# Kernel optimization log

Hardware: AMD Instinct MI355X
Metric: run time of the kernel (lower is better)

The kernel has to match this reference:

```python
import jax, jax.numpy as jnp
import numpy as np

D_MODEL = 2048
N_HEADS = 16
HEAD_DIM = D_MODEL // N_HEADS  # 128
MAX_T = 2048
ROPE_BASE = 10000.0


def _rope_tables(head_dim, max_t, base):
    inv = 1.0 / (base ** (np.arange(0, head_dim, 2, dtype=np.float32) / head_dim))
    t = np.arange(max_t, dtype=np.float32)
    fr = np.outer(t, inv)  # (T, head_dim//2)
    return jnp.asarray(np.cos(fr)), jnp.asarray(np.sin(fr))


def setup_inputs() -> dict:
    key = jax.random.key(0)
    k1, k2, k3 = jax.random.split(key, 3)
    B, T = 2, 2048
    x = jax.random.normal(k1, (B, T, D_MODEL), dtype=jnp.float32)
    Wqkv = jax.random.normal(k2, (3 * D_MODEL, D_MODEL), dtype=jnp.float32) * 0.02
    Wout = jax.random.normal(k3, (D_MODEL, D_MODEL), dtype=jnp.float32) * 0.02
    cos, sin = _rope_tables(HEAD_DIM, MAX_T, ROPE_BASE)
    rope_mask = jnp.arange(N_HEADS) < (N_HEADS // 2)  # first 8 heads RoPE, rest NoPE
    return {"x": x, "Wqkv": Wqkv, "Wout": Wout, "cos": cos, "sin": sin, "rope_mask": rope_mask}


def _apply_rope(t, cos, sin):
    # t: (B,H,T,hd); pairs are consecutive elements (x0,x1),(x2,x3),...
    B, H, T, hd = t.shape
    tr = t.reshape(B, H, T, hd // 2, 2)
    c = cos[:T][None, None, :, :]
    s = sin[:T][None, None, :, :]
    re = tr[..., 0] * c - tr[..., 1] * s
    im = tr[..., 0] * s + tr[..., 1] * c
    return jnp.stack([re, im], axis=-1).reshape(B, H, T, hd)


def reference(x, Wqkv, Wout, cos, sin, rope_mask):
    B, T, D = x.shape
    H = rope_mask.shape[0]
    hd = D // H
    qkv = x @ Wqkv.T  # (B,T,3D)
    q, k, v = jnp.split(qkv, 3, axis=-1)
    def heads(a):
        return a.reshape(B, T, H, hd).transpose(0, 2, 1, 3)  # (B,H,T,hd)
    q, k, v = heads(q), heads(k), heads(v)
    m = rope_mask[None, :, None, None]  # broadcast over (B,H,T,hd)
    q = jnp.where(m, _apply_rope(q, cos, sin), q)
    k = jnp.where(m, _apply_rope(k, cos, sin), k)
    scale = 1.0 / jnp.sqrt(jnp.asarray(hd, dtype=q.dtype))
    scores = jnp.einsum('bhtd,bhsd->bhts', q, k) * scale
    causal = jnp.tril(jnp.ones((T, T), dtype=bool))
    scores = jnp.where(causal[None, None], scores, jnp.asarray(-jnp.inf, dtype=scores.dtype))
    p = jax.nn.softmax(scores, axis=-1)
    out = jnp.einsum('bhts,bhsd->bhtd', p, v)
    out = out.transpose(0, 2, 1, 3).reshape(B, T, D)
    return out @ Wout.T
```

## Files before the change

### kernel.cpp

```cpp
#include <hip/hip_runtime.h>
#include <stdint.h>

typedef unsigned short u16;
typedef __attribute__((ext_vector_type(8))) short short8;
typedef __attribute__((ext_vector_type(4))) short s16x4;
typedef __attribute__((ext_vector_type(4))) float f32x4;
typedef __attribute__((ext_vector_type(16))) float f32x16;

__device__ __forceinline__ u16 f2bf(float f) {
  uint32_t x = __float_as_uint(f);
  x += 0x7fff + ((x >> 16) & 1);
  return (u16)(x >> 16);
}
__device__ __forceinline__ float bf2f(u16 u) {
  return __uint_as_float(((uint32_t)u) << 16);
}
__device__ __forceinline__ f32x4 mfma16(short8 a, short8 b, f32x4 c) {
  return __builtin_amdgcn_mfma_f32_16x16x32_bf16(a, b, c, 0, 0, 0);
}
__device__ __forceinline__ f32x16 mfma32(short8 a, short8 b, f32x16 c) {
  return __builtin_amdgcn_mfma_f32_32x32x16_bf16(a, b, c, 0, 0, 0);
}
__device__ __forceinline__ f32x4 mfma16k16(s16x4 a, s16x4 b, f32x4 c) {
  return __builtin_amdgcn_mfma_f32_16x16x16bf16_1k(a, b, c, 0, 0, 0);
}
__device__ __forceinline__ void gld16(const u16* g, u16* l) {
  __builtin_amdgcn_global_load_lds(
      (const __attribute__((address_space(1))) unsigned int*)g,
      (__attribute__((address_space(3))) unsigned int*)l, 16, 0, 0);
}
__device__ __forceinline__ float exp2a(float x) {
  float r;
  asm("v_exp_f32 %0, %1" : "=v"(r) : "v"(x));
  return r;
}

#define WAIT_VM(n) asm volatile("s_waitcnt vmcnt(" #n ")" ::: "memory")

__global__ __launch_bounds__(256) void cvt_all(const float* __restrict__ x,
                                               const float* __restrict__ wqkv,
                                               const float* __restrict__ wout,
                                               u16* __restrict__ xb,
                                               u16* __restrict__ wqkvb,
                                               u16* __restrict__ woutb) {
  long i = ((long)blockIdx.x * 256 + threadIdx.x) * 8;
  const float* s;
  u16* d;
  long off;
  if (i < 8388608) {
    s = x; d = xb; off = i;
  } else if (i < 20971520) {
    s = wqkv; d = wqkvb; off = i - 8388608;
  } else {
    s = wout; d = woutb; off = i - 20971520;
  }
  f32x4 a = *(const f32x4*)(s + off);
  f32x4 b = *(const f32x4*)(s + off + 4);
  short8 o;
#pragma unroll
  for (int j = 0; j < 4; j++) {
    o[j] = (short)f2bf(a[j]);
    o[j + 4] = (short)f2bf(b[j]);
  }
  *(short8*)(d + off) = o;
}

__global__ __launch_bounds__(512, 4) void gemm_qkv(const u16* __restrict__ A,
                                                   const u16* __restrict__ Bw,
                                                   u16* __restrict__ q3) {
  __shared__ __align__(16) u16 SA[12288];
  __shared__ __align__(16) u16 SB[18432];
  const int id = blockIdx.x;
  const int swz = (id & 7) * 128 + (id >> 3);
  const int by = swz & 31, bx = swz >> 5;
  const int m0 = by * 128, n0 = bx * 192;
  const int t = threadIdx.x, w = t >> 6, lane = t & 63;
  const int quad = lane >> 4, l15 = lane & 15;
  const int wm = w >> 2, wn = w & 3;
  const int rS = t >> 2, pS = t & 3;
  const int cS = (pS - (rS >> 1)) & 3;
  const size_t arowA = (size_t)(m0 + rS) * 2048 + cS * 8;
  const size_t arowB = (size_t)(n0 + rS) * 2048 + cS * 8;

  f32x4 acc[4][3] = {};
  const int pq = ((quad + (l15 >> 1)) & 3) * 8;

#define STAGE(KT, RS_)                                   \
  {                                                      \
    const u16* ga_ = A + arowA + (size_t)(KT) * 32;      \
    gld16(ga_, SA + (RS_)*4096 + t * 8);                 \
    const u16* gb_ = Bw + arowB + (size_t)(KT) * 32;     \
    u16* lb_ = SB + (RS_)*6144 + t * 8;                  \
    gld16(gb_, lb_);                                     \
    if (w < 4) gld16(gb_ + (size_t)128 * 2048, lb_ + 4096); \
  }

#define WAITQ                       \
  {                                 \
    if (w < 4) { WAIT_VM(3); }      \
    else       { WAIT_VM(2); }      \
  }

#define TILE(RC, RSS, TAU, DO_STAGE, WAIT)                                    \
  {                                                                           \
    const u16* Sa_ = SA + (RC)*4096;                                          \
    const u16* Sb_ = SB + (RC)*6144;                                          \
    if (DO_STAGE) STAGE((TAU) + 2, RSS);                                      \
    short8 af[4], bf[3];                                                      \
    _Pragma("unroll") for (int i = 0; i < 4; i++)                             \
        af[i] = *(const short8*)&Sa_[(wm * 64 + i * 16 + l15) * 32 + pq];     \
    _Pragma("unroll") for (int n = 0; n < 3; n++)                             \
        bf[n] = *(const short8*)&Sb_[(wn * 48 + n * 16 + l15) * 32 + pq];     \
    __builtin_amdgcn_s_setprio(1);                                            \
    _Pragma("unroll") for (int mi = 0; mi < 4; mi++)                          \
      _Pragma("unroll") for (int ni = 0; ni < 3; ni++)                        \
          acc[mi][ni] = mfma16(af[mi], bf[ni], acc[mi][ni]);                  \
    __builtin_amdgcn_s_setprio(0);                                            \
    WAIT;                                                                     \
    __builtin_amdgcn_s_barrier();                                             \
  }

  STAGE(0, 0);
  STAGE(1, 1);
  WAITQ;
  __builtin_amdgcn_s_barrier();

#pragma unroll 1
  for (int kt = 0; kt < 60; kt += 3) {
    TILE(0, 2, kt + 0, 1, WAITQ);
    TILE(1, 0, kt + 1, 1, WAITQ);
    TILE(2, 1, kt + 2, 1, WAITQ);
  }
  TILE(0, 2, 60, 1, WAITQ);
  TILE(1, 0, 61, 1, WAITQ);
  TILE(2, 1, 62, 0, WAIT_VM(0));
  TILE(0, 2, 63, 0, (void)0);
#undef TILE
#undef WAITQ
#undef STAGE

  const int bb = m0 >> 11, tt0 = m0 & 2047;
#pragma unroll
  for (int ni = 0; ni < 3; ni++) {
    const int gc = n0 + wn * 48 + ni * 16 + l15;
    const int which = gc >> 11;
    const int hh = (gc & 2047) >> 7, di = gc & 127;
    if (which == 2) {
      u16* vb = q3 + 16777216 + ((size_t)(bb * 16 + hh) * 128 + di) * 2048;
#pragma unroll
      for (int mi = 0; mi < 4; mi++) {
        const int tloc = tt0 + wm * 64 + mi * 16 + quad * 4;
        s16x4 st;
#pragma unroll
        for (int r = 0; r < 4; r++) st[r] = (short)f2bf(acc[mi][ni][r]);
        *(s16x4*)(vb + tloc) = st;
      }
    } else {
      const float sc = (which == 0) ? 0.1275174f : 1.0f;
      u16* qb = q3 + (size_t)which * 8388608 +
                ((size_t)(bb * 16 + hh) * 2048) * 128 + di;
#pragma unroll
      for (int mi = 0; mi < 4; mi++) {
        const int tloc = tt0 + wm * 64 + mi * 16 + quad * 4;
#pragma unroll
        for (int r = 0; r < 4; r++)
          qb[(size_t)(tloc + r) * 128] = f2bf(acc[mi][ni][r] * sc);
      }
    }
  }
}

template <int EPI>
__global__ __launch_bounds__(256) void gemm_bt(const u16* __restrict__ A,
                                               const u16* __restrict__ B,
                                               int K, void* __restrict__ Cv, int N) {
  __shared__ __align__(16) u16 SMEM[8448];
  u16* As = SMEM;
  u16* Bs = SMEM + 4096;
  const int m0 = blockIdx.y * 128, n0 = blockIdx.x * 128;
  const int t = threadIdx.x, w = t >> 6, lane = t & 63;
  const int l31 = lane & 31, half = lane >> 5;
  const int rb = (w >> 1) * 64, cb = (w & 1) * 64;
  f32x16 acc[2][2] = {};
  const int rowS = w * 16 + (lane >> 2);
  const int cS = ((lane & 3) - (rowS >> 1)) & 3;
  const u16* ag = A + (size_t)(m0 + rowS) * K + cS * 8;
  const u16* bg = B + (size_t)(n0 + rowS) * K + cS * 8;
  u16* al = As + w * 512 + lane * 8;
  u16* bl = Bs + w * 512 + lane * 8;
  const size_t rowskip = (size_t)64 * K;
  const int p0 = ((0 * 2 + half + (l31 >> 1)) & 3) * 8;
  const int p1 = ((1 * 2 + half + (l31 >> 1)) & 3) * 8;
  for (int k0 = 0; k0 < K; k0 += 32) {
    __syncthreads();
    gld16(ag, al);
    gld16(ag + rowskip, al + 2048);
    gld16(bg, bl);
    gld16(bg + rowskip, bl + 2048);
    ag += 32;
    bg += 32;
    __syncthreads();
    short8 af[2][2], bfr[2][2];
#pragma unroll
    for (int mi = 0; mi < 2; mi++) {
      af[mi][0] = *(const short8*)&As[(rb + mi * 32 + l31) * 32 + p0];
      af[mi][1] = *(const short8*)&As[(rb + mi * 32 + l31) * 32 + p1];
    }
#pragma unroll
    for (int ni = 0; ni < 2; ni++) {
      bfr[ni][0] = *(const short8*)&Bs[(cb + ni * 32 + l31) * 32 + p0];
      bfr[ni][1] = *(const short8*)&Bs[(cb + ni * 32 + l31) * 32 + p1];
    }
#pragma unroll
    for (int kh = 0; kh < 2; kh++)
#pragma unroll
      for (int mi = 0; mi < 2; mi++)
#pragma unroll
        for (int ni = 0; ni < 2; ni++)
          acc[mi][ni] = mfma32(af[mi][kh], bfr[ni][kh], acc[mi][ni]);
  }

  if (EPI == 0) {
    const int which = n0 >> 11;
    const int hh = (n0 & 2047) >> 7;
    const int bb = m0 >> 11, tt0 = m0 & 2047;
    u16* q3 = (u16*)Cv;
    if (which == 2) {
      u16* vbase = q3 + 16777216 + ((size_t)(bb * 16 + hh) * 128) * 2048;
#pragma unroll
      for (int mi = 0; mi < 2; mi++)
#pragma unroll
        for (int ni = 0; ni < 2; ni++) {
          int di = cb + ni * 32 + l31;
          int trow = tt0 + rb + mi * 32 + half * 4;
#pragma unroll
          for (int rg2 = 0; rg2 < 4; rg2++) {
            s16x4 st;
#pragma unroll
            for (int j = 0; j < 4; j++) st[j] = (short)f2bf(acc[mi][ni][rg2 * 4 + j]);
            *(s16x4*)(vbase + (size_t)di * 2048 + trow + rg2 * 8) = st;
          }
        }
    } else {
      const float sc = (which == 0) ? 0.1275174f : 1.0f;
      u16* base = q3 + (size_t)which * 8388608 + ((size_t)(bb * 16 + hh) * 2048) * 128;
#pragma unroll
      for (int mi = 0; mi < 2; mi++)
#pragma unroll
        for (int ni = 0; ni < 2; ni++) {
          int di = cb + ni * 32 + l31;
          int trow = tt0 + rb + mi * 32 + half * 4;
#pragma unroll
          for (int reg = 0; reg < 16; reg++) {
            int tt = trow + (reg & 3) + 8 * (reg >> 2);
            base[(size_t)tt * 128 + di] = f2bf(acc[mi][ni][reg] * sc);
          }
        }
    }
  } else {
    float* Es = (float*)SMEM;
    float* C = (float*)Cv;
#pragma unroll
    for (int r = 0; r < 4; r++) {
      __syncthreads();
      if ((w >> 1) == (r >> 1)) {
        const int mi = r & 1;
#pragma unroll
        for (int ni = 0; ni < 2; ni++) {
          int col = cb + ni * 32 + l31;
#pragma unroll
          for (int reg = 0; reg < 16; reg++) {
            int lrow = (reg & 3) + 8 * (reg >> 2) + half * 4;
            Es[lrow * 132 + col] = acc[mi][ni][reg];
          }
        }
      }
      __syncthreads();
#pragma unroll
      for (int it = 0; it < 4; it++) {
        int idx = it * 256 + t;
        int row = idx >> 5, ch = idx & 31;
        f32x4 vv = *(const f32x4*)&Es[row * 132 + ch * 4];
        *(f32x4*)&C[(size_t)(m0 + r * 32 + row) * N + n0 + ch * 4] = vv;
      }
    }
  }
}

__global__ __launch_bounds__(256) void rope_k(u16* __restrict__ q, u16* __restrict__ k,
                                              const float* __restrict__ cosT,
                                              const float* __restrict__ sinT) {
  int t = threadIdx.x;
  int row = blockIdx.x * 4 + (t >> 6);
  int i = t & 63;
  int b = row >> 14;
  int h = (row >> 11) & 7;
  int tp = row & 2047;
  size_t base = ((size_t)((b * 16 + h) * 2048 + tp)) * 128 + 2 * i;
  float c = cosT[tp * 64 + i], s = sinT[tp * 64 + i];
  {
    uint32_t u = *(uint32_t*)(q + base);
    float x0 = bf2f((u16)(u & 0xffff)), x1 = bf2f((u16)(u >> 16));
    float re = x0 * c - x1 * s, im = x0 * s + x1 * c;
    *(uint32_t*)(q + base) = (uint32_t)f2bf(re) | ((uint32_t)f2bf(im) << 16);
  }
  {
    uint32_t u = *(uint32_t*)(k + base);
    float x0 = bf2f((u16)(u & 0xffff)), x1 = bf2f((u16)(u >> 16));
    float re = x0 * c - x1 * s, im = x0 * s + x1 * c;
    *(uint32_t*)(k + base) = (uint32_t)f2bf(re) | ((uint32_t)f2bf(im) << 16);
  }
}

__global__ __launch_bounds__(256, 2) void attn_k(const u16* __restrict__ qh,
                                                 const u16* __restrict__ kh,
                                                 const u16* __restrict__ vTh,
                                                 u16* __restrict__ attno) {
  __shared__ __align__(16) u16 Ks[16384];
  __shared__ __align__(16) u16 Vt[16384];
  const int i = blockIdx.x;
  const int jj = i & 255, half = i >> 8;
  const int bh = jj >> 3, t8 = jj & 7;
  const int qt = half ? (15 - t8) : t8;
  const int q0 = qt * 128;
  const int t = threadIdx.x, w = t >> 6, lane = t & 63;
  const int quad = lane >> 4, l15 = lane & 15;
  const size_t bhoff = (size_t)bh * 262144;

  short8 qb[2][4];
  {
    const u16* qp = qh + bhoff + (size_t)(q0 + w * 32 + l15) * 128 + quad * 8;
#pragma unroll
    for (int qq = 0; qq < 2; qq++)
#pragma unroll
      for (int ks = 0; ks < 4; ks++)
        qb[qq][ks] = *(const short8*)(qp + qq * 2048 + ks * 32);
  }
  f32x4 of[2][8] = {};
  float mst[2] = {-1e30f, -1e30f}, lst[2] = {0.f, 0.f};
  const int nkt = 2 * qt + 2;
  const int wq0 = q0 + w * 32;

#define ASTAGE(KT, BUF)                                                        \
  {                                                                            \
    const int k0_ = (KT) * 64;                                                 \
    _Pragma("unroll") for (int it = 0; it < 4; it++) {                         \
      int L = it * 256 + t;                                                    \
      int key = L >> 4, c = L & 15;                                            \
      gld16(kh + bhoff + (size_t)(k0_ + key) * 128 + ((c ^ (key & 15)) * 8),   \
            Ks + (BUF)*8192 + (size_t)L * 8);                                  \
    }                                                                          \
    _Pragma("unroll") for (int it = 0; it < 4; it++) {                         \
      int L = it * 256 + t;                                                    \
      int d = L >> 3, c = L & 7;                                               \
      gld16(vTh + bhoff + (size_t)d * 2048 + k0_ + ((c ^ (d & 7)) * 8),        \
            Vt + (BUF)*8192 + (size_t)L * 8);                                  \
    }                                                                          \
  }

  ASTAGE(0, 0);
#pragma unroll 1
  for (int kt = 0; kt < nkt; kt++) {
    const int buf = kt & 1;
    const int k0 = kt * 64;
    __builtin_amdgcn_s_barrier();
    if (kt + 1 < nkt) {
      ASTAGE(kt + 1, buf ^ 1);
      WAIT_VM(8);
    } else {
      WAIT_VM(0);
    }
    __builtin_amdgcn_s_barrier();
    if (k0 <= wq0 + 31) {
      const u16* Kb = Ks + buf * 8192;
      const u16* Vb = Vt + buf * 8192;
      f32x4 sacc[2][4];
#pragma unroll
      for (int qq = 0; qq < 2; qq++)
#pragma unroll
        for (int kk = 0; kk < 4; kk++) sacc[qq][kk] = (f32x4){0.f, 0.f, 0.f, 0.f};
#pragma unroll
      for (int kk = 0; kk < 4; kk++) {
        short8 kf[4];
#pragma unroll
        for (int ks = 0; ks < 4; ks++)
          kf[ks] = *(const short8*)&Kb[(kk * 16 + l15) * 128 + ((ks * 4 + quad) ^ l15) * 8];
        __builtin_amdgcn_s_setprio(1);
#pragma unroll
        for (int qq = 0; qq < 2; qq++)
#pragma unroll
          for (int ks = 0; ks < 4; ks++)
            sacc[qq][kk] = mfma16(kf[ks], qb[qq][ks], sacc[qq][kk]);
        __builtin_amdgcn_s_setprio(0);
      }
      const bool needmask = (k0 + 63 > wq0);
      s16x4 pf[2][4];
      float alpha[2];
#pragma unroll
      for (int qq = 0; qq < 2; qq++) {
        const int qg = wq0 + qq * 16 + l15;
        if (needmask) {
#pragma unroll
          for (int kk = 0; kk < 4; kk++)
#pragma unroll
            for (int rg = 0; rg < 4; rg++)
              if (k0 + kk * 16 + quad * 4 + rg > qg) sacc[qq][kk][rg] = -1e30f;
        }
        float pm = -1e30f;
#pragma unroll
        for (int kk = 0; kk < 4; kk++)
#pragma unroll
          for (int rg = 0; rg < 4; rg++) pm = fmaxf(pm, sacc[qq][kk][rg]);
        pm = fmaxf(pm, __shfl_xor(pm, 16));
        pm = fmaxf(pm, __shfl_xor(pm, 32));
        float mnew = fmaxf(mst[qq], pm);
        alpha[qq] = exp2a(mst[qq] - mnew);
        mst[qq] = mnew;
        float ps = 0.f;
#pragma unroll
        for (int kk = 0; kk < 4; kk++) {
          float e0 = exp2a(sacc[qq][kk][0] - mnew);
          float e1 = exp2a(sacc[qq][kk][1] - mnew);
          float e2 = exp2a(sacc[qq][kk][2] - mnew);
          float e3 = exp2a(sacc[qq][kk][3] - mnew);
          ps += (e0 + e1) + (e2 + e3);
          pf[qq][kk][0] = (short)f2bf(e0);
          pf[qq][kk][1] = (short)f2bf(e1);
          pf[qq][kk][2] = (short)f2bf(e2);
          pf[qq][kk][3] = (short)f2bf(e3);
        }
        ps += __shfl_xor(ps, 16);
        ps += __shfl_xor(ps, 32);
        lst[qq] = lst[qq] * alpha[qq] + ps;
      }
#pragma unroll
      for (int qq = 0; qq < 2; qq++) {
        if (!__all(alpha[qq] == 1.0f)) {
          float a = alpha[qq];
#pragma unroll
          for (int df = 0; df < 8; df++) of[qq][df] *= a;
        }
      }
#pragma unroll
      for (int df = 0; df < 8; df++) {
        s16x4 vf[4];
#pragma unroll
        for (int kk = 0; kk < 4; kk++)
          vf[kk] = *(const s16x4*)&Vb[(df * 16 + l15) * 64 +
                                      ((kk * 2 + (quad >> 1)) ^ (l15 & 7)) * 8 +
                                      (quad & 1) * 4];
        __builtin_amdgcn_s_setprio(1);
#pragma unroll
        for (int qq = 0; qq < 2; qq++)
#pragma unroll
          for (int kk = 0; kk < 4; kk++)
            of[qq][df] = mfma16k16(vf[kk], pf[qq][kk], of[qq][df]);
        __builtin_amdgcn_s_setprio(0);
      }
    }
  }
#undef ASTAGE
  const int b = bh >> 4, h = bh & 15;
#pragma unroll
  for (int qq = 0; qq < 2; qq++) {
    float linv = 1.0f / lst[qq];
    const size_t row = (size_t)(b * 2048 + q0 + w * 32 + qq * 16 + l15);
#pragma unroll
    for (int df = 0; df < 8; df++) {
      s16x4 o;
#pragma unroll
      for (int rg = 0; rg < 4; rg++) o[rg] = (short)f2bf(of[qq][df][rg] * linv);
      *(s16x4*)(attno + row * 2048 + h * 128 + df * 16 + quad * 4) = o;
    }
  }
}

extern "C" void kernel_launch(void* const* d_in, const int* in_sizes, int n_in,
                              void* d_out, int out_size, void* d_ws, size_t ws_size,
                              hipStream_t stream) {
  const float* x = (const float*)d_in[0];
  const float* Wqkv = (const float*)d_in[1];
  const float* Wout = (const float*)d_in[2];
  const float* cosT = (const float*)d_in[3];
  const float* sinT = (const float*)d_in[4];
  float* out = (float*)d_out;
  char* ws = (char*)d_ws;
  u16* qkvh = (u16*)(ws + 0);
  u16* woutb = (u16*)(ws + 50331648);
  u16* xb = (u16*)(ws + 58720256);
  u16* wqkvb = (u16*)(ws + 75497472);
  u16* attno = wqkvb;

  cvt_all<<<12288, 256, 0, stream>>>(x, Wqkv, Wout, xb, wqkvb, woutb);
  gemm_qkv<<<1024, 512, 0, stream>>>(xb, wqkvb, qkvh);
  rope_k<<<8192, 256, 0, stream>>>(qkvh, qkvh + 8388608, cosT, sinT);
  attn_k<<<512, 256, 0, stream>>>(qkvh, qkvh + 8388608, qkvh + 16777216, attno);
  gemm_bt<1><<<dim3(16, 32), 256, 0, stream>>>(attno, woutb, 2048, (void*)out, 2048);
}
```

Before: 390.4 us.

## Replace output projection GEMM with triple-buffered 512-thread pipelined kernel

Replaces the generic gemm_bt output projection with a dedicated gemm_out kernel. The new kernel uses 8 waves and 16x16x32 MFMAs. It triple-buffers LDS with async global-to-LDS loads issued two tiles ahead, waits with vmcnt, and raises wave priority around the MFMA block. It also swizzles the block index for L2 locality. The goal is to hide global load latency behind compute, where the old loop used one buffer with two barriers per k-step. The cost is higher LDS use per block and hardcoded dimensions.

After: 386.5 us. No clear change (-1.0%).

```diff
diff --git a/kernel.cpp b/kernel.cpp
--- a/kernel.cpp
+++ b/kernel.cpp
@@ -17,9 +17,6 @@
 }
 __device__ __forceinline__ f32x4 mfma16(short8 a, short8 b, f32x4 c) {
   return __builtin_amdgcn_mfma_f32_16x16x32_bf16(a, b, c, 0, 0, 0);
-}
-__device__ __forceinline__ f32x16 mfma32(short8 a, short8 b, f32x16 c) {
-  return __builtin_amdgcn_mfma_f32_32x32x16_bf16(a, b, c, 0, 0, 0);
 }
 __device__ __forceinline__ f32x4 mfma16k16(s16x4 a, s16x4 b, f32x4 c) {
   return __builtin_amdgcn_mfma_f32_16x16x16bf16_1k(a, b, c, 0, 0, 0);
@@ -170,119 +167,94 @@
   }
 }
 
-template <int EPI>
-__global__ __launch_bounds__(256) void gemm_bt(const u16* __restrict__ A,
-                                               const u16* __restrict__ B,
-                                               int K, void* __restrict__ Cv, int N) {
-  __shared__ __align__(16) u16 SMEM[8448];
-  u16* As = SMEM;
-  u16* Bs = SMEM + 4096;
-  const int m0 = blockIdx.y * 128, n0 = blockIdx.x * 128;
+__global__ __launch_bounds__(512, 4) void gemm_out(const u16* __restrict__ A,
+                                                   const u16* __restrict__ Bw,
+                                                   float* __restrict__ C) {
+  __shared__ __align__(16) u16 SA[12288];
+  __shared__ __align__(16) u16 SB[12288];
+  const int id = blockIdx.x;
+  const int swz = (id & 7) * 64 + (id >> 3);
+  const int by = swz & 31, bx = swz >> 5;
+  const int m0 = by * 128, n0 = bx * 128;
   const int t = threadIdx.x, w = t >> 6, lane = t & 63;
-  const int l31 = lane & 31, half = lane >> 5;
-  const int rb = (w >> 1) * 64, cb = (w & 1) * 64;
-  f32x16 acc[2][2] = {};
-  const int rowS = w * 16 + (lane >> 2);
-  const int cS = ((lane & 3) - (rowS >> 1)) & 3;
-  const u16* ag = A + (size_t)(m0 + rowS) * K + cS * 8;
-  const u16* bg = B + (size_t)(n0 + rowS) * K + cS * 8;
-  u16* al = As + w * 512 + lane * 8;
-  u16* bl = Bs + w * 512 + lane * 8;
-  const size_t rowskip = (size_t)64 * K;
-  const int p0 = ((0 * 2 + half + (l31 >> 1)) & 3) * 8;
-  const int p1 = ((1 * 2 + half + (l31 >> 1)) & 3) * 8;
-  for (int k0 = 0; k0 < K; k0 += 32) {
+  const int quad = lane >> 4, l15 = lane & 15;
+  const int wm = w >> 2, wn = w & 3;
+  const int rS = t >> 2, pS = t & 3;
+  const int cS = (pS - (rS >> 1)) & 3;
+  const size_t arowA = (size_t)(m0 + rS) * 2048 + cS * 8;
+  const size_t arowB = (size_t)(n0 + rS) * 2048 + cS * 8;
+
+  f32x4 acc[4][2] = {};
+  const int pq = ((quad + (l15 >> 1)) & 3) * 8;
+
+#define STAGE(KT, RS_)                                   \
+  {                                                      \
+    gld16(A + arowA + (size_t)(KT) * 32, SA + (RS_)*4096 + t * 8); \
+    gld16(Bw + arowB + (size_t)(KT) * 32, SB + (RS_)*4096 + t * 8); \
+  }
+
+#define TILE(RC, RSS, TAU, DO_STAGE, WAIT)                                    \
+  {                                                                           \
+    const u16* Sa_ = SA + (RC)*4096;                                          \
+    const u16* Sb_ = SB + (RC)*4096;                                          \
+    if (DO_STAGE) STAGE((TAU) + 2, RSS);                                      \
+    short8 af[4], bf[2];                                                      \
+    _Pragma("unroll") for (int i = 0; i < 4; i++)                             \
+        af[i] = *(const short8*)&Sa_[(wm * 64 + i * 16 + l15) * 32 + pq];     \
+    _Pragma("unroll") for (int n = 0; n < 2; n++)                             \
+        bf[n] = *(const short8*)&Sb_[(wn * 32 + n * 16 + l15) * 32 + pq];     \
+    __builtin_amdgcn_s_setprio(1);                                            \
+    _Pragma("unroll") for (int mi = 0; mi < 4; mi++)                          \
+      _Pragma("unroll") for (int ni = 0; ni < 2; ni++)                        \
+          acc[mi][ni] = mfma16(af[mi], bf[ni], acc[mi][ni]);                  \
+    __builtin_amdgcn_s_setprio(0);                                            \
+    WAIT;                                                                     \
+    __builtin_amdgcn_s_barrier();                                             \
+  }
+
+  STAGE(0, 0);
+  STAGE(1, 1);
+  WAIT_VM(2);
+  __builtin_amdgcn_s_barrier();
+
+#pragma unroll 1
+  for (int kt = 0; kt < 60; kt += 3) {
+    TILE(0, 2, kt + 0, 1, WAIT_VM(2));
+    TILE(1, 0, kt + 1, 1, WAIT_VM(2));
+    TILE(2, 1, kt + 2, 1, WAIT_VM(2));
+  }
+  TILE(0, 2, 60, 1, WAIT_VM(2));
+  TILE(1, 0, 61, 1, WAIT_VM(2));
+  TILE(2, 1, 62, 0, WAIT_VM(0));
+  TILE(0, 2, 63, 0, (void)0);
+#undef TILE
+#undef STAGE
+
+  float* Es = (float*)SA;
+#pragma unroll
+  for (int r = 0; r < 4; r++) {
     __syncthreads();
-    gld16(ag, al);
-    gld16(ag + rowskip, al + 2048);
-    gld16(bg, bl);
-    gld16(bg + rowskip, bl + 2048);
-    ag += 32;
-    bg += 32;
+    if (wm == (r >> 1)) {
+      const int mib = (r & 1) * 2;
+#pragma unroll
+      for (int ni = 0; ni < 2; ni++) {
+        const int col = wn * 32 + ni * 16 + l15;
+#pragma unroll
+        for (int mo = 0; mo < 2; mo++)
+#pragma unroll
+          for (int rg = 0; rg < 4; rg++) {
+            const int lrow = mo * 16 + quad * 4 + rg;
+            Es[lrow * 132 + col] = acc[mib + mo][ni][rg];
+          }
+      }
+    }
     __syncthreads();
-    short8 af[2][2], bfr[2][2];
-#pragma unroll
-    for (int mi = 0; mi < 2; mi++) {
-      af[mi][0] = *(const short8*)&As[(rb + mi * 32 + l31) * 32 + p0];
-      af[mi][1] = *(const short8*)&As[(rb + mi * 32 + l31) * 32 + p1];
-    }
-#pragma unroll
-    for (int ni = 0; ni < 2; ni++) {
-      bfr[ni][0] = *(const short8*)&Bs[(cb + ni * 32 + l31) * 32 + p0];
-      bfr[ni][1] = *(const short8*)&Bs[(cb + ni * 32 + l31) * 32 + p1];
-    }
-#pragma unroll
-    for (int kh = 0; kh < 2; kh++)
-#pragma unroll
-      for (int mi = 0; mi < 2; mi++)
-#pragma unroll
-        for (int ni = 0; ni < 2; ni++)
-          acc[mi][ni] = mfma32(af[mi][kh], bfr[ni][kh], acc[mi][ni]);
-  }
-
-  if (EPI == 0) {
-    const int which = n0 >> 11;
-    const int hh = (n0 & 2047) >> 7;
-    const int bb = m0 >> 11, tt0 = m0 & 2047;
-    u16* q3 = (u16*)Cv;
-    if (which == 2) {
-      u16* vbase = q3 + 16777216 + ((size_t)(bb * 16 + hh) * 128) * 2048;
-#pragma unroll
-      for (int mi = 0; mi < 2; mi++)
-#pragma unroll
-        for (int ni = 0; ni < 2; ni++) {
-          int di = cb + ni * 32 + l31;
-          int trow = tt0 + rb + mi * 32 + half * 4;
-#pragma unroll
-          for (int rg2 = 0; rg2 < 4; rg2++) {
-            s16x4 st;
-#pragma unroll
-            for (int j = 0; j < 4; j++) st[j] = (short)f2bf(acc[mi][ni][rg2 * 4 + j]);
-            *(s16x4*)(vbase + (size_t)di * 2048 + trow + rg2 * 8) = st;
-          }
-        }
-    } else {
-      const float sc = (which == 0) ? 0.1275174f : 1.0f;
-      u16* base = q3 + (size_t)which * 8388608 + ((size_t)(bb * 16 + hh) * 2048) * 128;
-#pragma unroll
-      for (int mi = 0; mi < 2; mi++)
-#pragma unroll
-        for (int ni = 0; ni < 2; ni++) {
-          int di = cb + ni * 32 + l31;
-          int trow = tt0 + rb + mi * 32 + half * 4;
-#pragma unroll
-          for (int reg = 0; reg < 16; reg++) {
-            int tt = trow + (reg & 3) + 8 * (reg >> 2);
-            base[(size_t)tt * 128 + di] = f2bf(acc[mi][ni][reg] * sc);
-          }
-        }
-    }
-  } else {
-    float* Es = (float*)SMEM;
-    float* C = (float*)Cv;
-#pragma unroll
-    for (int r = 0; r < 4; r++) {
-      __syncthreads();
-      if ((w >> 1) == (r >> 1)) {
-        const int mi = r & 1;
-#pragma unroll
-        for (int ni = 0; ni < 2; ni++) {
-          int col = cb + ni * 32 + l31;
-#pragma unroll
-          for (int reg = 0; reg < 16; reg++) {
-            int lrow = (reg & 3) + 8 * (reg >> 2) + half * 4;
-            Es[lrow * 132 + col] = acc[mi][ni][reg];
-          }
-        }
-      }
-      __syncthreads();
-#pragma unroll
-      for (int it = 0; it < 4; it++) {
-        int idx = it * 256 + t;
-        int row = idx >> 5, ch = idx & 31;
-        f32x4 vv = *(const f32x4*)&Es[row * 132 + ch * 4];
-        *(f32x4*)&C[(size_t)(m0 + r * 32 + row) * N + n0 + ch * 4] = vv;
-      }
+#pragma unroll
+    for (int it = 0; it < 2; it++) {
+      const int idx = it * 512 + t;
+      const int row = idx >> 5, ch = idx & 31;
+      f32x4 vv = *(const f32x4*)&Es[row * 132 + ch * 4];
+      *(f32x4*)&C[(size_t)(m0 + r * 32 + row) * 2048 + n0 + ch * 4] = vv;
     }
   }
 }
@@ -495,5 +467,5 @@
   gemm_qkv<<<1024, 512, 0, stream>>>(xb, wqkvb, qkvh);
   rope_k<<<8192, 256, 0, stream>>>(qkvh, qkvh + 8388608, cosT, sinT);
   attn_k<<<512, 256, 0, stream>>>(qkvh, qkvh + 8388608, qkvh + 16777216, attno);
-  gemm_bt<1><<<dim3(16, 32), 256, 0, stream>>>(attno, woutb, 2048, (void*)out, 2048);
-}
+  gemm_out<<<512, 512, 0, stream>>>(attno, woutb, out);
+}
```
